# Performance work log

Hardware: AMD Instinct MI355X
Metric: run time of the kernel (lower is better)

## Reference

```python
import jax, jax.numpy as jnp
import numpy as np

B, L, P = 65536, 512, 96
E_LIN, E = 14, 16
FFT = 512
TEMP = 0.07
K = 2
EPS = 1e-5


def setup_inputs() -> dict:
    key = jax.random.key(0)
    k0, k1, k2 = jax.random.split(key, 3)
    x = jax.random.normal(k0, (B, L), dtype=jnp.float32)
    Wg = jax.random.normal(k1, (E, FFT // 2), dtype=jnp.float32) * 0.02
    bg = jnp.zeros((E,), dtype=jnp.float32)
    Wr = jax.random.normal(k2, (E_LIN, P, L), dtype=jnp.float32) * 0.02
    br = jnp.zeros((E_LIN, P), dtype=jnp.float32)
    return {"x": x, "Wg": Wg, "bg": bg, "Wr": Wr, "br": br}


def _periodogram(x):
    # x: [B, L] -> normalized power spectrum [B, FFT//2]
    x0 = x - jnp.mean(x, axis=1, keepdims=True)
    dft = jnp.fft.fft(x0, n=FFT, axis=1) / np.float32(np.sqrt(FFT))
    dft = dft[:, : FFT // 2]
    I = dft.real ** 2 + dft.imag ** 2
    s = jnp.sum(I, axis=1, keepdims=True)
    s = jnp.where(s == 0, jnp.ones_like(s), s)
    return I / s


def reference(x, Wg, bg, Wr, br):
    # gating (eval mode: no noise, divide by temperature)
    I = _periodogram(x)                                  # [B, F/2]
    gate = (I @ Wg.T + bg) / TEMP                        # [B, E]
    topv, topi = jax.lax.top_k(gate, K)                  # [B, K]
    gates = jax.nn.softmax(topv, axis=1)                 # [B, K]

    # RLinear experts: RevIN(norm) -> Linear -> RevIN(denorm); stats detached
    mu = jax.lax.stop_gradient(jnp.mean(x, axis=1, keepdims=True))        # [B,1]
    sd = jax.lax.stop_gradient(jnp.sqrt(jnp.var(x, axis=1, keepdims=True) + EPS))
    xn = (x - mu) / sd                                   # [B, L]
    yr = jnp.einsum('bl,epl->bep', xn, Wr) + br          # [B, E_LIN, P]
    yr = yr * sd[:, :, None] + mu[:, :, None]

    mean_out = jnp.broadcast_to(jnp.mean(x, axis=1, keepdims=True), (x.shape[0], P))[:, None, :]
    naive_out = jnp.broadcast_to(x[:, -1:], (x.shape[0], P))[:, None, :]

    eo = jnp.concatenate([yr, mean_out, naive_out], axis=1)   # [B, E, P]
    sel = jnp.take_along_axis(eo, topi[:, :, None], axis=1)   # [B, K, P]
    out = jnp.sum(gates[:, :, None] * sel, axis=1)            # [B, P]
    return out
```

## Files before the change

### kernel.cpp

```cpp
#include <hip/hip_runtime.h>
#include <math.h>

#define NB_B 65536
#define NL   512
#define NP   96
#define NE   16
#define NEL  14
#define NF   256
#define TEMP_INV (1.0f/0.07f)
#define TAU  1e-5f
#define PI_D 3.14159265358979323846
#define MAXCHK 1536

typedef __attribute__((ext_vector_type(8))) short bf16x8;
typedef __attribute__((ext_vector_type(4))) float f32x4;


#define WS_PCNT     0
#define WS_HOLES    16384
#define WS_PBASE    32768
#define WS_FLAGCNT  33792
#define WS_NCHK     33824
#define WS_HOLECNT  33840
#define WS_FLAG     33856
#define WS_SSUM     296000
#define WS_WGT      301376
#define WS_BGT      317760
#define WS_TWD      319872
#define WS_REC      328064
#define WS_HDR      590208
#define WS_RIDX     1638784
#define WS_WRB      1933696
#define WS_DESC     3506560
#define WS_XB16     3512704
#define WS_XB16_END 70621568

__device__ __forceinline__ unsigned short f2bf(float f) {
    unsigned u = __float_as_uint(f);
    unsigned r = (u + 0x7fffu + ((u >> 16) & 1u)) >> 16;
    return (unsigned short)r;
}

__global__ __launch_bounds__(256) void k_prep(
    const float* __restrict__ Wg, const float* __restrict__ bg,
    const float* __restrict__ Wr,
    float* __restrict__ Ssum, float* __restrict__ WgE, float* __restrict__ bgT,
    double2* __restrict__ twd,
    int* __restrict__ pcnt, int* __restrict__ flagcnt, int* __restrict__ holecnt,
    ushort4* __restrict__ Wrb, int perm)
{
    int g = blockIdx.x * 256 + threadIdx.x;
    {
        ushort4 o = make_ushort4(0, 0, 0, 0);
        if (g < NEL * NP * NL / 4) {
            float4 v;
            if (perm) {
                int row = g >> 7, sq = g & 127;
                int ll = sq >> 1, kb = (sq & 1) * 4;
                const float* wr = Wr + (size_t)row * NL + ll;
                v.x = wr[(kb + 0) * 64]; v.y = wr[(kb + 1) * 64];
                v.z = wr[(kb + 2) * 64]; v.w = wr[(kb + 3) * 64];
            } else {
                v = ((const float4*)Wr)[g];
            }
            o.x = f2bf(v.x); o.y = f2bf(v.y); o.z = f2bf(v.z); o.w = f2bf(v.w);
        }
        Wrb[g] = o;
    }
    if (g < NEL * NP * 8) {
        int row = g >> 3, seg = g & 7;
        const float4* w = (const float4*)(Wr + (size_t)row * NL + seg * 64);
        float s = 0.f;
#pragma unroll
        for (int i = 0; i < 16; i++) { float4 v = w[i]; s += v.x + v.y + v.z + v.w; }
        s += __shfl_xor(s, 1); s += __shfl_xor(s, 2); s += __shfl_xor(s, 4);
        if (seg == 0) Ssum[row] = s;
    }
    if (g < 4096) {
        int c = g & 3, e = (g >> 2) & 15, f4 = g >> 6;
        WgE[g] = Wg[e * NF + f4 * 4 + c] * TEMP_INV;
    }
    if (g < 512) {
        double a = -2.0 * PI_D * (double)g / 512.0;
        twd[g] = make_double2(cos(a), sin(a));
    }
    if (g < 256) pcnt[g << 4] = 0;
    if (g < NE) bgT[g] = bg[g] * TEMP_INV;
    if (g == 300) *flagcnt = 0;
    if (g == 301) *holecnt = 0;
}

__global__ __launch_bounds__(256, 4) void k_gate(
    const float* __restrict__ x,
    const float4* __restrict__ WgE4, const float* __restrict__ bgT,
    int* __restrict__ rec, float4* __restrict__ hdr,
    int* __restrict__ flaglist, int* __restrict__ flagcnt,
    int* __restrict__ pcnt, unsigned short* __restrict__ xb16, int bofs)
{
    __shared__ __align__(16) float2 s_z[4][576];
    float* s_Iv = (float*)&s_z[0][0];

    const int t = threadIdx.x;
    const int wv = t >> 6, l = t & 63;
    const int b0 = (bofs + blockIdx.x) * 8 + wv * 2;

    const float th = -6.283185307179586f / 512.0f;
    const float R2 = 0.70710678118654752f;
    float s1, c1; __sincosf((float)l * th, &s1, &c1);
    float s2, c2; __sincosf((float)(2 * l) * th, &s2, &c2);
    float sw0, cw0; __sincosf((float)((l & 31) << 3) * th, &sw0, &cw0);
    float sw1, cw1; __sincosf((float)((l & 15) << 4) * th, &sw1, &cw1);
    float sw2, cw2; __sincosf((float)((l & 7) << 5) * th, &sw2, &cw2);
    float2 tw0[4];
    tw0[0] = make_float2(c1, s1);
    tw0[1] = make_float2(R2 * (c1 + s1), R2 * (s1 - c1));
    tw0[2] = make_float2(s1, -c1);
    tw0[3] = make_float2(tw0[1].y, -tw0[1].x);
    float2 tw1[2];
    tw1[0] = make_float2(c2, s2);
    tw1[1] = make_float2(s2, -c2);
    const float2 w2 = make_float2(c2 * c2 - s2 * s2, 2.f * c2 * s2);
    float2 wst[5];
    wst[0] = make_float2(cw0, sw0);
    wst[1] = make_float2(cw1, sw1);
    wst[2] = make_float2(cw2, sw2);
    {
        int j2 = l & 3;
        float cc3 = (j2 == 0) ? 1.f : (j2 == 1) ? R2 : (j2 == 2) ? 0.f : -R2;
        float ss3 = (j2 == 0) ? 0.f : (j2 == 2) ? -1.f : -R2;
        wst[3] = make_float2(cc3, ss3);
    }
    wst[4] = (l & 1) ? make_float2(0.f, -1.f) : make_float2(1.f, 0.f);

    const float* xa = x + (size_t)b0 * NL;
    const float* xb = xa + NL;
    float xr[8], xi[8];
#pragma unroll
    for (int k = 0; k < 8; k++) { xr[k] = xa[k * 64 + l]; xi[k] = xb[k * 64 + l]; }
    const float last_a = __shfl(xr[7], 63);
    const float last_b = __shfl(xi[7], 63);

    if (xb16) {
        unsigned pa_[4], pb_[4];
#pragma unroll
        for (int j = 0; j < 4; j++) {
            asm("v_cvt_pk_bf16_f32 %0, %1, %2" : "=v"(pa_[j]) : "v"(xr[2 * j]), "v"(xr[2 * j + 1]));
            asm("v_cvt_pk_bf16_f32 %0, %1, %2" : "=v"(pb_[j]) : "v"(xi[2 * j]), "v"(xi[2 * j + 1]));
        }
        *(uint4*)(xb16 + (size_t)b0 * NL + l * 8)       = *(uint4*)pa_;
        *(uint4*)(xb16 + (size_t)(b0 + 1) * NL + l * 8) = *(uint4*)pb_;
    }

#pragma unroll
    for (int k = 0; k < 4; k++) {
        float2 w = tw0[k];
        float ur = xr[k], ui = xi[k], vr = xr[k + 4], vi = xi[k + 4];
        xr[k] = ur + vr; xi[k] = ui + vi;
        float dr = ur - vr, di = ui - vi;
        xr[k + 4] = dr * w.x - di * w.y; xi[k + 4] = dr * w.y + di * w.x;
    }
    {
        const int kk[4] = {0, 1, 4, 5};
#pragma unroll
        for (int g2 = 0; g2 < 4; g2++) {
            int k = kk[g2];
            float2 w = tw1[k & 1];
            float ur = xr[k], ui = xi[k], vr = xr[k + 2], vi = xi[k + 2];
            xr[k] = ur + vr; xi[k] = ui + vi;
            float dr = ur - vr, di = ui - vi;
            xr[k + 2] = dr * w.x - di * w.y; xi[k + 2] = dr * w.y + di * w.x;
        }
    }
    {
#pragma unroll
        for (int k = 0; k < 8; k += 2) {
            float ur = xr[k], ui = xi[k], vr = xr[k + 1], vi = xi[k + 1];
            xr[k] = ur + vr; xi[k] = ui + vi;
            float dr = ur - vr, di = ui - vi;
            xr[k + 1] = dr * w2.x - di * w2.y; xi[k + 1] = dr * w2.y + di * w2.x;
        }
    }
#pragma unroll
    for (int st = 3; st < 8; st++) {
        const int half = 256 >> st;
        const float2 w = wst[st - 3];
        const bool up = (l & half) != 0;
        const float sg = up ? -1.f : 1.f;
        const float cc = up ? w.x : 1.f;
        const float ss = up ? w.y : 0.f;
#pragma unroll
        for (int k = 0; k < 8; k++) {
            float pr = __shfl_xor(xr[k], half);
            float pi = __shfl_xor(xi[k], half);
            float tr = fmaf(sg, xr[k], pr);
            float ti = fmaf(sg, xi[k], pi);
            xr[k] = tr * cc - ti * ss;
            xi[k] = tr * ss + ti * cc;
        }
    }
    {
        const float sg = (l & 1) ? -1.f : 1.f;
#pragma unroll
        for (int k = 0; k < 8; k++) {
            float pr = __shfl_xor(xr[k], 1);
            float pi = __shfl_xor(xi[k], 1);
            xr[k] = fmaf(sg, xr[k], pr);
            xi[k] = fmaf(sg, xi[k], pi);
        }
    }

#pragma unroll
    for (int k = 0; k < 8; k++) {
        int i = k * 64 + l;
        s_z[wv][i + (i >> 3)] = make_float2(xr[k], xi[k]);
    }

    float Ia[4], Ib[4];
    float psa = 0.f, psb = 0.f;
#pragma unroll
    for (int j = 0; j < 4; j++) {
        int f = (l << 2) | j;
        int i1_ = (int)(__brev((unsigned)f) >> 23);
        int i2_ = (int)(__brev((unsigned)((512 - f) & 511)) >> 23);
        float2 z1 = s_z[wv][i1_ + (i1_ >> 3)];
        float2 z2 = s_z[wv][i2_ + (i2_ >> 3)];
        float pr_ = z1.x + z2.x, qm = z1.y - z2.y;
        float qp = z1.y + z2.y, pm = z1.x - z2.x;
        float va = pr_ * pr_ + qm * qm;
        float vb = qp * qp + pm * pm;
        if (f == 0) { va = 0.f; vb = 0.f; }
        Ia[j] = va; Ib[j] = vb;
        psa += va; psb += vb;
    }
#pragma unroll
    for (int m = 1; m < 64; m <<= 1) {
        psa += __shfl_xor(psa, m); psb += __shfl_xor(psb, m);
    }
    const float psa_raw = psa, psb_raw = psb;
    if (psa == 0.f) psa = 1.f;
    if (psb == 0.f) psb = 1.f;
    const float inv_a = 1.f / psa, inv_b = 1.f / psb;

    const float2 Z0   = s_z[wv][0];
    const float2 Z256 = s_z[wv][1];

    float* wI = s_Iv + wv * 1152;
    const int io = (l << 2) + ((l >> 4) << 2);
    *(float4*)(wI + io)       = make_float4(Ia[0], Ia[1], Ia[2], Ia[3]);
    *(float4*)(wI + 272 + io) = make_float4(Ib[0], Ib[1], Ib[2], Ib[3]);

    const int e16 = l & 15, cq = l >> 4;
    const float bgv = bgT[e16];
    float accA = 0.f, accB = 0.f;
    const float* rA = wI + cq * 68;
    const float* rB = rA + 272;
#pragma unroll 4
    for (int jj = 0; jj < 16; jj++) {
        float4 ia = *(const float4*)(rA + 4 * jj);
        float4 ib = *(const float4*)(rB + 4 * jj);
        float4 w = WgE4[(cq * 16 + jj) * 16 + e16];
        accA += ia.x * w.x + ia.y * w.y + ia.z * w.z + ia.w * w.w;
        accB += ib.x * w.x + ib.y * w.y + ib.z * w.z + ib.w * w.w;
    }
    accA += __shfl_xor(accA, 16); accA += __shfl_xor(accA, 32);
    accB += __shfl_xor(accB, 16); accB += __shfl_xor(accB, 32);

    float v = ((l & 16) ? accB * inv_b : accA * inv_a) + bgv;

    float b0v = v; int b0i = e16;
#pragma unroll
    for (int m = 1; m < 16; m <<= 1) {
        float ov = __shfl_xor(b0v, m); int oi = __shfl_xor(b0i, m);
        if (ov > b0v || (ov == b0v && oi < b0i)) { b0v = ov; b0i = oi; }
    }
    float v1 = (e16 == b0i) ? -1e30f : v;
    float b1v = v1; int b1i = e16;
#pragma unroll
    for (int m = 1; m < 16; m <<= 1) {
        float ov = __shfl_xor(b1v, m); int oi = __shfl_xor(b1i, m);
        if (ov > b1v || (ov == b1v && oi < b1i)) { b1v = ov; b1i = oi; }
    }
    float v2 = (e16 == b1i) ? -1e30f : v1;
    float b2v = v2;
#pragma unroll
    for (int m = 1; m < 16; m <<= 1) {
        float ov = __shfl_xor(b2v, m);
        b2v = fmaxf(b2v, ov);
    }

    if (l == 0 || l == 16) {
        const int r = l >> 4;
        const int b = b0 + r;
        const float mu = (r ? Z0.y : Z0.x) * (1.f / 512.f);
        const float Jv = r ? Z256.y : Z256.x;
        const float ps = r ? psb_raw : psa_raw;
        const float sd = sqrtf((0.5f * ps + Jv * Jv) * (1.f / 262144.f) + 1e-5f);
        const float last = r ? last_b : last_a;
        const float w0 = 1.f / (1.f + expf(b1v - b0v));
        const int pid = b0i * 16 + b1i;
        const int lo = atomicAdd(&pcnt[pid << 4], 1);
        rec[b] = (pid << 24) | lo;
        hdr[b] = make_float4(mu, sd, last, w0);
        if (b1v - b2v < TAU) {
            int pos = atomicAdd(flagcnt, 1);
            flaglist[pos] = b;
        }
    }
}

__global__ __launch_bounds__(256) void k_refine(
    const float* __restrict__ x, const double2* __restrict__ twd,
    const float* __restrict__ Wg, const float* __restrict__ bg,
    int* __restrict__ rec, float4* __restrict__ hdr,
    const int* __restrict__ flaglist, const int* __restrict__ flagcnt,
    int* __restrict__ pcnt, int* __restrict__ holes, int* __restrict__ holecnt)
{
    __shared__ double s_x[512];
    __shared__ double s_I[256];
    __shared__ double s_red[16];
    __shared__ double s_g[16];
    const int nf = *flagcnt;
    const int t = threadIdx.x;
    const int wid = t >> 6, lane = t & 63;
    for (int fi = blockIdx.x; fi < nf; fi += gridDim.x) {
        const int b = flaglist[fi];
        const float* xp = x + (size_t)b * NL;
        double v0 = (double)xp[t], v1 = (double)xp[t + 256];
        double lsum = v0 + v1;
        for (int m = 1; m < 64; m <<= 1) lsum += __shfl_xor(lsum, m);
        if (lane == 0) s_red[wid] = lsum;
        __syncthreads();
        double mu = (s_red[0] + s_red[1] + s_red[2] + s_red[3]) * (1.0 / 512.0);
        s_x[t] = v0 - mu; s_x[t + 256] = v1 - mu;
        __syncthreads();
        double2 w = twd[t];
        double pr = 1.0, pi = 0.0, cr = 0.0, ci = 0.0;
        for (int n = 0; n < 512; n++) {
            double xv = s_x[n];
            cr += xv * pr; ci += xv * pi;
            double t2 = pr * w.x - pi * w.y;
            pi = pr * w.y + pi * w.x;
            pr = t2;
        }
        double I = cr * cr + ci * ci;
        s_I[t] = I;
        double ls = I;
        for (int m = 1; m < 64; m <<= 1) ls += __shfl_xor(ls, m);
        if (lane == 0) s_red[8 + wid] = ls;
        __syncthreads();
        double stot = s_red[8] + s_red[9] + s_red[10] + s_red[11];
        if (stot == 0.0) stot = 1.0;
        if (t < 16) {
            double acc = 0.0;
            const float* wrow = Wg + t * NF;
            for (int f = 0; f < NF; f++) acc += s_I[f] * (double)wrow[f];
            s_g[t] = (acc / stot + (double)bg[t]) * (1.0 / 0.07);
        }
        __syncthreads();
        if (t == 0) {
            double c0 = -1e300, c1 = -1e300; int j0 = 0, j1 = 0;
            for (int i = 0; i < 16; i++) {
                double v = s_g[i];
                if (v > c0) { c1 = c0; j1 = j0; c0 = v; j0 = i; }
                else if (v > c1) { c1 = v; j1 = i; }
            }
            double e1 = exp(c1 - c0);
            float w0f = (float)(1.0 / (1.0 + e1));
            int newpid = j0 * 16 + j1;
            int oldrec = rec[b];
            int oldpid = (int)(((unsigned)oldrec) >> 24);
            if (newpid == oldpid) {
                ((float*)(hdr + b))[3] = w0f;
            } else {
                int pos = atomicAdd(holecnt, 1);
                if (pos < 4096) {
                    int nlo = atomicAdd(&pcnt[newpid << 4], 1);
                    rec[b] = (newpid << 24) | nlo;
                    holes[pos] = oldrec;
                    ((float*)(hdr + b))[3] = w0f;
                }
            }
        }
        __syncthreads();
    }
}

__global__ __launch_bounds__(256) void k_scan(
    const int* __restrict__ pcnt, int* __restrict__ pbase,
    int* __restrict__ desc, int* __restrict__ nchk)
{
    __shared__ int s[256], c[256];
    const int t = threadIdx.x;
    const int n = pcnt[t << 4];
    s[t] = n;
    c[t] = (n + 63) >> 6;
    __syncthreads();
    for (int off = 1; off < 256; off <<= 1) {
        int v1 = (t >= off) ? s[t - off] : 0;
        int v2 = (t >= off) ? c[t - off] : 0;
        __syncthreads();
        s[t] += v1; c[t] += v2;
        __syncthreads();
    }
    int excl = t ? s[t - 1] : 0;
    int cexcl = t ? c[t - 1] : 0;
    pbase[t] = excl;
    int myc = (n + 63) >> 6;
    for (int j = 0; j < myc; j++) desc[cexcl + j] = (t << 16) | j;
    if (t == 255) *nchk = cexcl + myc;
}

__global__ __launch_bounds__(256) void k_scatter(
    const int* __restrict__ rec, const int* __restrict__ pbase,
    int* __restrict__ ridx,
    const int* __restrict__ holes, const int* __restrict__ holecnt)
{
    const int t = threadIdx.x;
    const int b = blockIdx.x * 256 + t;
    unsigned v = (unsigned)rec[b];
    ridx[pbase[v >> 24] + (v & 0xFFFFFF)] = b;
    if (blockIdx.x == 0) {
        int nh = *holecnt; if (nh > 4096) nh = 4096;
        for (int h = t; h < nh; h += 256) {
            unsigned hv = (unsigned)holes[h];
            ridx[pbase[hv >> 24] + (hv & 0xFFFFFF)] = -1;
        }
    }
}

__global__ __launch_bounds__(256) void k_gemm2(
    const unsigned short* __restrict__ xb16,
    const unsigned short* __restrict__ Wrb,
    const float* __restrict__ br, const float* __restrict__ Ssum,
    const float4* __restrict__ hdr, float* __restrict__ out,
    const int* __restrict__ pcnt, const int* __restrict__ pbase,
    const int* __restrict__ ridx,
    const int* __restrict__ desc, const int* __restrict__ nchk)
{
    __shared__ __align__(16) unsigned short sB[2][2][96 * 68];
    __shared__ int    s_idx[64];
    __shared__ float4 s_hdr[64];
    __shared__ float  s_br[2][96], s_S[2][96];
    if ((int)blockIdx.x >= *nchk) return;
    const int d = desc[blockIdx.x];
    const int pid = d >> 16, cc = d & 0xffff;
    const int n = pcnt[pid << 4];
    const int base = pbase[pid];
    const int i0 = pid >> 4, i1 = pid & 15;
    const int t = threadIdx.x;
    const int lane = t & 63, wv = t >> 6;
    const int quad = lane >> 4, l16 = lane & 15;
    if (t < 96) {
        s_br[0][t] = (i0 < NEL) ? br[i0 * NP + t] : 0.f;
        s_S [0][t] = (i0 < NEL) ? Ssum[i0 * NP + t] : 0.f;
        s_br[1][t] = (i1 < NEL) ? br[i1 * NP + t] : 0.f;
        s_S [1][t] = (i1 < NEL) ? Ssum[i1 * NP + t] : 0.f;
    }
    if (t < 64) {
        int g = cc * 64 + t;
        bool vld = g < n;
        int row = vld ? ridx[base + g] : -1;
        s_idx[t] = row;
        s_hdr[t] = (row >= 0) ? hdr[row] : make_float4(0.f, 0.f, 0.f, 0.f);
    }

    const unsigned short* wb[2];
    wb[0] = Wrb + (size_t)i0 * NP * NL;
    wb[1] = Wrb + (size_t)i1 * NP * NL;
    unsigned boff[6]; int bpos[6], bex[6];
#pragma unroll
    for (int it = 0; it < 6; it++) {
        int ex = (it >= 3);
        int fl = t + (it - 3 * ex) * 256;
        int p = fl >> 3, kg = fl & 7;
        bex[it] = ex;
        boff[it] = (unsigned)(p * NL + kg * 8);
        bpos[it] = p * 68 + kg * 8;
    }

    bf16x8 bR[6];
#pragma unroll
    for (int it = 0; it < 6; it++) bR[it] = *(const bf16x8*)(wb[bex[it]] + boff[it]);
#pragma unroll
    for (int it = 0; it < 6; it++) *(bf16x8*)(&sB[0][bex[it]][bpos[it]]) = bR[it];
    __syncthreads();

    int arow = s_idx[wv * 16 + l16]; if (arow < 0) arow = 0;
    const unsigned short* aP = xb16 + (size_t)arow * NL + quad * 8;

    f32x4 acc[2][6];
#pragma unroll
    for (int ex = 0; ex < 2; ex++)
#pragma unroll
        for (int j = 0; j < 6; j++) acc[ex][j] = (f32x4){0.f, 0.f, 0.f, 0.f};

    bf16x8 a0 = *(const bf16x8*)(aP);
    bf16x8 a1 = *(const bf16x8*)(aP + 32);

    int cb = 0;
    for (int kb = 0; kb < NL; kb += 64) {
        const int kn = kb + 64;
        bf16x8 an0, an1;
        if (kn < NL) {
#pragma unroll
            for (int it = 0; it < 6; it++)
                bR[it] = *(const bf16x8*)(wb[bex[it]] + boff[it] + kn);
            an0 = *(const bf16x8*)(aP + kn);
            an1 = *(const bf16x8*)(aP + kn + 32);
        }
#pragma unroll
        for (int ks = 0; ks < 2; ks++)
#pragma unroll
            for (int ex = 0; ex < 2; ex++)
#pragma unroll
                for (int nt = 0; nt < 6; nt++) {
                    bf16x8 bf = *(const bf16x8*)(&sB[cb][ex][(nt * 16 + l16) * 68 + ks * 32 + quad * 8]);
                    acc[ex][nt] = __builtin_amdgcn_mfma_f32_16x16x32_bf16(
                        ks ? a1 : a0, bf, acc[ex][nt], 0, 0, 0);
                }
        if (kn < NL) {
#pragma unroll
            for (int it = 0; it < 6; it++) *(bf16x8*)(&sB[cb ^ 1][bex[it]][bpos[it]]) = bR[it];
            __syncthreads();
            cb ^= 1;
            a0 = an0; a1 = an1;
        }
    }

#pragma unroll
    for (int i = 0; i < 4; i++) {
        int rloc = wv * 16 + quad * 4 + i;
        int row = s_idx[rloc];
        if (row >= 0) {
            float4 h = s_hdr[rloc];
            float mu = h.x, sd = h.y, last = h.z, w0 = h.w, w1 = 1.f - w0;
            float* orow = out + (size_t)row * NP;
#pragma unroll
            for (int nt = 0; nt < 6; nt++) {
                int p = nt * 16 + l16;
                float v0 = (i0 < NEL) ? (mu + s_br[0][p] * sd - mu * s_S[0][p] + acc[0][nt][i])
                                      : (i0 == NEL ? mu : last);
                float v1 = (i1 < NEL) ? (mu + s_br[1][p] * sd - mu * s_S[1][p] + acc[1][nt][i])
                                      : (i1 == NEL ? mu : last);
                orow[p] = w0 * v0 + w1 * v1;
            }
        }
    }
}

__global__ __launch_bounds__(256) void k_gemm_f32(
    const float* __restrict__ x,
    const unsigned short* __restrict__ Wrb,
    const float* __restrict__ br, const float* __restrict__ Ssum,
    const float4* __restrict__ hdr, float* __restrict__ out,
    const int* __restrict__ pcnt, const int* __restrict__ pbase,
    const int* __restrict__ ridx,
    const int* __restrict__ desc, const int* __restrict__ nchk)
{
    __shared__ __align__(16) unsigned short sA[64 * 72];
    __shared__ __align__(16) unsigned short sB[2][96 * 72];
    __shared__ int    s_idx[64];
    __shared__ float4 s_hdr[64];
    __shared__ float  s_br[2][96], s_S[2][96];
    if ((int)blockIdx.x >= *nchk) return;
    const int d = desc[blockIdx.x];
    const int pid = d >> 16, cc = d & 0xffff;
    const int n = pcnt[pid << 4];
    const int base = pbase[pid];
    const int i0 = pid >> 4, i1 = pid & 15;
    const int t = threadIdx.x;
    const int lane = t & 63, wv = t >> 6;
    const int quad = lane >> 4, l16 = lane & 15;
    const int ar = t >> 2, asub = t & 3;
    if (t < 96) {
        s_br[0][t] = (i0 < NEL) ? br[i0 * NP + t] : 0.f;
        s_S [0][t] = (i0 < NEL) ? Ssum[i0 * NP + t] : 0.f;
        s_br[1][t] = (i1 < NEL) ? br[i1 * NP + t] : 0.f;
        s_S [1][t] = (i1 < NEL) ? Ssum[i1 * NP + t] : 0.f;
    }
    if (t < 64) {
        int g = cc * 64 + t;
        bool vld = g < n;
        int row = vld ? ridx[base + g] : -1;
        s_idx[t] = row;
        s_hdr[t] = (row >= 0) ? hdr[row] : make_float4(0.f, 0.f, 0.f, 0.f);
    }
    __syncthreads();

    f32x4 acc[2][6];
#pragma unroll
    for (int ex = 0; ex < 2; ex++)
#pragma unroll
        for (int j = 0; j < 6; j++) acc[ex][j] = (f32x4){0.f, 0.f, 0.f, 0.f};

    int rr = s_idx[ar]; if (rr < 0) rr = 0;

    unsigned boff[6];
    unsigned short* bdst[6];
    const unsigned short* wb[2];
    wb[0] = Wrb + (size_t)i0 * NP * NL;
    wb[1] = Wrb + (size_t)i1 * NP * NL;
    int bex[6];
#pragma unroll
    for (int it = 0; it < 6; it++) {
        int ex = (it >= 3);
        int fl = t + (it - 3 * ex) * 256;
        int p = fl >> 3, kg = fl & 7;
        bex[it] = ex;
        boff[it] = (unsigned)(p * NL + kg * 8);
        bdst[it] = &sB[ex][p * 72 + kg * 8];
    }
    unsigned short* adst = sA + ar * 72 + asub * 16;
    const float* xrowf = x + (size_t)rr * NL + asub * 16;

    float4 fA[4]; bf16x8 bR[6];
#pragma unroll
    for (int i = 0; i < 4; i++) fA[i] = ((const float4*)xrowf)[i];
#pragma unroll
    for (int it = 0; it < 6; it++) bR[it] = *(const bf16x8*)(wb[bex[it]] + boff[it]);

    for (int kb = 0; kb < NL; kb += 64) {
        unsigned short tmp[16];
#pragma unroll
        for (int i = 0; i < 4; i++) {
            float4 v = fA[i];
            tmp[i * 4 + 0] = f2bf(v.x); tmp[i * 4 + 1] = f2bf(v.y);
            tmp[i * 4 + 2] = f2bf(v.z); tmp[i * 4 + 3] = f2bf(v.w);
        }
        *(bf16x8*)adst       = *(bf16x8*)tmp;
        *(bf16x8*)(adst + 8) = *(bf16x8*)(tmp + 8);
#pragma unroll
        for (int it = 0; it < 6; it++) *(bf16x8*)bdst[it] = bR[it];
        __syncthreads();

        const int kn = kb + 64;
        if (kn < NL) {
#pragma unroll
            for (int i = 0; i < 4; i++) fA[i] = ((const float4*)(xrowf + kn))[i];
#pragma unroll
            for (int it = 0; it < 6; it++)
                bR[it] = *(const bf16x8*)(wb[bex[it]] + boff[it] + kn);
        }

#pragma unroll
        for (int ks = 0; ks < 2; ks++) {
            bf16x8 af = *(const bf16x8*)(sA + (wv * 16 + l16) * 72 + ks * 32 + quad * 8);
#pragma unroll
            for (int ex = 0; ex < 2; ex++)
#pragma unroll
                for (int nt = 0; nt < 6; nt++) {
                    bf16x8 bf = *(const bf16x8*)(&sB[ex][(nt * 16 + l16) * 72 + ks * 32 + quad * 8]);
                    acc[ex][nt] = __builtin_amdgcn_mfma_f32_16x16x32_bf16(af, bf, acc[ex][nt], 0, 0, 0);
                }
        }
        __syncthreads();
    }
#pragma unroll
    for (int i = 0; i < 4; i++) {
        int rloc = wv * 16 + quad * 4 + i;
        int row = s_idx[rloc];
        if (row >= 0) {
            float4 h = s_hdr[rloc];
            float mu = h.x, sd = h.y, last = h.z, w0 = h.w, w1 = 1.f - w0;
            float* orow = out + (size_t)row * NP;
#pragma unroll
            for (int nt = 0; nt < 6; nt++) {
                int p = nt * 16 + l16;
                float v0 = (i0 < NEL) ? (mu + s_br[0][p] * sd - mu * s_S[0][p] + acc[0][nt][i])
                                      : (i0 == NEL ? mu : last);
                float v1 = (i1 < NEL) ? (mu + s_br[1][p] * sd - mu * s_S[1][p] + acc[1][nt][i])
                                      : (i1 == NEL ? mu : last);
                orow[p] = w0 * v0 + w1 * v1;
            }
        }
    }
}

extern "C" void kernel_launch(void* const* d_in, const int* in_sizes, int n_in,
                              void* d_out, int out_size, void* d_ws, size_t ws_size,
                              hipStream_t stream)
{
    const float* x  = (const float*)d_in[0];
    const float* Wg = (const float*)d_in[1];
    const float* bg = (const float*)d_in[2];
    const float* Wr = (const float*)d_in[3];
    const float* br = (const float*)d_in[4];
    float* out = (float*)d_out;
    char* ws = (char*)d_ws;

    int*     pcnt     = (int*)(ws + WS_PCNT);
    int*     holes    = (int*)(ws + WS_HOLES);
    int*     pbase    = (int*)(ws + WS_PBASE);
    int*     flagcnt  = (int*)(ws + WS_FLAGCNT);
    int*     nchk     = (int*)(ws + WS_NCHK);
    int*     holecnt  = (int*)(ws + WS_HOLECNT);
    int*     flaglist = (int*)(ws + WS_FLAG);
    float*   Ssum     = (float*)(ws + WS_SSUM);
    float*   WgE      = (float*)(ws + WS_WGT);
    float*   bgT      = (float*)(ws + WS_BGT);
    double2* twd      = (double2*)(ws + WS_TWD);
    int*     rec      = (int*)(ws + WS_REC);
    float4*  hdr      = (float4*)(ws + WS_HDR);
    int*     ridx     = (int*)(ws + WS_RIDX);
    unsigned short* Wrb = (unsigned short*)(ws + WS_WRB);
    int*     desc     = (int*)(ws + WS_DESC);

    const int use_xb = (ws_size >= (size_t)WS_XB16_END);
    unsigned short* xb16 = use_xb ? (unsigned short*)(ws + WS_XB16) : (unsigned short*)0;

    k_prep<<<dim3(768), dim3(256), 0, stream>>>(Wg, bg, Wr, Ssum, WgE, bgT, twd,
                                                pcnt, flagcnt, holecnt,
                                                (ushort4*)Wrb, use_xb);
    k_gate<<<dim3(NB_B / 16), dim3(256), 0, stream>>>(x, (const float4*)WgE, bgT,
                                                      rec, hdr, flaglist, flagcnt, pcnt,
                                                      xb16, 0);
    k_gate<<<dim3(NB_B / 16), dim3(256), 0, stream>>>(x, (const float4*)WgE, bgT,
                                                      rec, hdr, flaglist, flagcnt, pcnt,
                                                      xb16, NB_B / 16);
    k_refine<<<dim3(512), dim3(256), 0, stream>>>(x, twd, Wg, bg, rec, hdr,
                                                  flaglist, flagcnt, pcnt, holes, holecnt);
    k_scan<<<dim3(1), dim3(256), 0, stream>>>(pcnt, pbase, desc, nchk);
    k_scatter<<<dim3(NB_B / 256), dim3(256), 0, stream>>>(rec, pbase, ridx, holes, holecnt);
    if (use_xb)
        k_gemm2<<<dim3(MAXCHK), dim3(256), 0, stream>>>(xb16, Wrb, br, Ssum, hdr, out,
                                                        pcnt, pbase, ridx, desc, nchk);
    else
        k_gemm_f32<<<dim3(MAXCHK), dim3(256), 0, stream>>>(x, Wrb, br, Ssum, hdr, out,
                                                           pcnt, pbase, ridx, desc, nchk);
}
```

Baseline: 306.7 us.

## Single-buffer gemm LDS, XCD-aware block remap, nontemporal loads/stores, merge gate launches

The grouped expert GEMM drops LDS double buffering in favour of a single buffer per expert, halving shared memory at the cost of an extra barrier per k-step. Chunk indices are remapped so consecutive descriptors spread across the 8 XCDs. Activation, header and output accesses use nontemporal hints to avoid polluting cache. The two half-batch gate launches are fused into one launch.

```diff
diff --git a/kernel.cpp b/kernel.cpp
--- a/kernel.cpp
+++ b/kernel.cpp
@@ -14,6 +14,7 @@
 
 typedef __attribute__((ext_vector_type(8))) short bf16x8;
 typedef __attribute__((ext_vector_type(4))) float f32x4;
+typedef __attribute__((ext_vector_type(4))) unsigned int u32x4;
 
 
 #define WS_PCNT     0
@@ -39,6 +40,14 @@
     unsigned u = __float_as_uint(f);
     unsigned r = (u + 0x7fffu + ((u >> 16) & 1u)) >> 16;
     return (unsigned short)r;
+}
+__device__ __forceinline__ bf16x8 ldnt_bf16x8(const unsigned short* p) {
+    u32x4 v = __builtin_nontemporal_load((const u32x4*)p);
+    union { u32x4 u; bf16x8 h; } c; c.u = v; return c.h;
+}
+__device__ __forceinline__ float4 ldnt_f4(const float4* p) {
+    u32x4 v = __builtin_nontemporal_load((const u32x4*)p);
+    union { u32x4 u; float4 f; } c; c.u = v; return c.f;
 }
 
 __global__ __launch_bounds__(256) void k_prep(
@@ -95,14 +104,14 @@
     const float4* __restrict__ WgE4, const float* __restrict__ bgT,
     int* __restrict__ rec, float4* __restrict__ hdr,
     int* __restrict__ flaglist, int* __restrict__ flagcnt,
-    int* __restrict__ pcnt, unsigned short* __restrict__ xb16, int bofs)
+    int* __restrict__ pcnt, unsigned short* __restrict__ xb16)
 {
     __shared__ __align__(16) float2 s_z[4][576];
     float* s_Iv = (float*)&s_z[0][0];
 
     const int t = threadIdx.x;
     const int wv = t >> 6, l = t & 63;
-    const int b0 = (bofs + blockIdx.x) * 8 + wv * 2;
+    const int b0 = blockIdx.x * 8 + wv * 2;
 
     const float th = -6.283185307179586f / 512.0f;
     const float R2 = 0.70710678118654752f;
@@ -428,7 +437,7 @@
     }
 }
 
-__global__ __launch_bounds__(256) void k_gemm2(
+__global__ __launch_bounds__(256) void k_gemm3(
     const unsigned short* __restrict__ xb16,
     const unsigned short* __restrict__ Wrb,
     const float* __restrict__ br, const float* __restrict__ Ssum,
@@ -437,12 +446,13 @@
     const int* __restrict__ ridx,
     const int* __restrict__ desc, const int* __restrict__ nchk)
 {
-    __shared__ __align__(16) unsigned short sB[2][2][96 * 68];
+    __shared__ __align__(16) unsigned short sB[2][96 * 68];
     __shared__ int    s_idx[64];
     __shared__ float4 s_hdr[64];
     __shared__ float  s_br[2][96], s_S[2][96];
-    if ((int)blockIdx.x >= *nchk) return;
-    const int d = desc[blockIdx.x];
+    const int lb = (int)(blockIdx.x % 8) * (MAXCHK / 8) + (int)(blockIdx.x / 8);
+    if (lb >= *nchk) return;
+    const int d = desc[lb];
     const int pid = d >> 16, cc = d & 0xffff;
     const int n = pcnt[pid << 4];
     const int base = pbase[pid];
@@ -461,7 +471,7 @@
         bool vld = g < n;
         int row = vld ? ridx[base + g] : -1;
         s_idx[t] = row;
-        s_hdr[t] = (row >= 0) ? hdr[row] : make_float4(0.f, 0.f, 0.f, 0.f);
+        s_hdr[t] = (row >= 0) ? ldnt_f4(hdr + row) : make_float4(0.f, 0.f, 0.f, 0.f);
     }
 
     const unsigned short* wb[2];
@@ -481,8 +491,6 @@
     bf16x8 bR[6];
 #pragma unroll
     for (int it = 0; it < 6; it++) bR[it] = *(const bf16x8*)(wb[bex[it]] + boff[it]);
-#pragma unroll
-    for (int it = 0; it < 6; it++) *(bf16x8*)(&sB[0][bex[it]][bpos[it]]) = bR[it];
     __syncthreads();
 
     int arow = s_idx[wv * 16 + l16]; if (arow < 0) arow = 0;
@@ -494,35 +502,36 @@
 #pragma unroll
         for (int j = 0; j < 6; j++) acc[ex][j] = (f32x4){0.f, 0.f, 0.f, 0.f};
 
-    bf16x8 a0 = *(const bf16x8*)(aP);
-    bf16x8 a1 = *(const bf16x8*)(aP + 32);
-
-    int cb = 0;
+    bf16x8 a0 = ldnt_bf16x8(aP);
+    bf16x8 a1 = ldnt_bf16x8(aP + 32);
+
     for (int kb = 0; kb < NL; kb += 64) {
+#pragma unroll
+        for (int it = 0; it < 6; it++) *(bf16x8*)(&sB[bex[it]][bpos[it]]) = bR[it];
+        __syncthreads();
+
         const int kn = kb + 64;
         bf16x8 an0, an1;
         if (kn < NL) {
 #pragma unroll
             for (int it = 0; it < 6; it++)
                 bR[it] = *(const bf16x8*)(wb[bex[it]] + boff[it] + kn);
-            an0 = *(const bf16x8*)(aP + kn);
-            an1 = *(const bf16x8*)(aP + kn + 32);
-        }
+            an0 = ldnt_bf16x8(aP + kn);
+            an1 = ldnt_bf16x8(aP + kn + 32);
+        }
+
 #pragma unroll
         for (int ks = 0; ks < 2; ks++)
 #pragma unroll
             for (int ex = 0; ex < 2; ex++)
 #pragma unroll
                 for (int nt = 0; nt < 6; nt++) {
-                    bf16x8 bf = *(const bf16x8*)(&sB[cb][ex][(nt * 16 + l16) * 68 + ks * 32 + quad * 8]);
+                    bf16x8 bf = *(const bf16x8*)(&sB[ex][(nt * 16 + l16) * 68 + ks * 32 + quad * 8]);
                     acc[ex][nt] = __builtin_amdgcn_mfma_f32_16x16x32_bf16(
                         ks ? a1 : a0, bf, acc[ex][nt], 0, 0, 0);
                 }
         if (kn < NL) {
-#pragma unroll
-            for (int it = 0; it < 6; it++) *(bf16x8*)(&sB[cb ^ 1][bex[it]][bpos[it]]) = bR[it];
             __syncthreads();
-            cb ^= 1;
             a0 = an0; a1 = an1;
         }
     }
@@ -542,7 +551,7 @@
                                       : (i0 == NEL ? mu : last);
                 float v1 = (i1 < NEL) ? (mu + s_br[1][p] * sd - mu * s_S[1][p] + acc[1][nt][i])
                                       : (i1 == NEL ? mu : last);
-                orow[p] = w0 * v0 + w1 * v1;
+                __builtin_nontemporal_store(w0 * v0 + w1 * v1, &orow[p]);
             }
         }
     }
@@ -711,18 +720,14 @@
     k_prep<<<dim3(768), dim3(256), 0, stream>>>(Wg, bg, Wr, Ssum, WgE, bgT, twd,
                                                 pcnt, flagcnt, holecnt,
                                                 (ushort4*)Wrb, use_xb);
-    k_gate<<<dim3(NB_B / 16), dim3(256), 0, stream>>>(x, (const float4*)WgE, bgT,
-                                                      rec, hdr, flaglist, flagcnt, pcnt,
-                                                      xb16, 0);
-    k_gate<<<dim3(NB_B / 16), dim3(256), 0, stream>>>(x, (const float4*)WgE, bgT,
-                                                      rec, hdr, flaglist, flagcnt, pcnt,
-                                                      xb16, NB_B / 16);
+    k_gate<<<dim3(NB_B / 8), dim3(256), 0, stream>>>(x, (const float4*)WgE, bgT,
+                                                     rec, hdr, flaglist, flagcnt, pcnt, xb16);
     k_refine<<<dim3(512), dim3(256), 0, stream>>>(x, twd, Wg, bg, rec, hdr,
                                                   flaglist, flagcnt, pcnt, holes, holecnt);
     k_scan<<<dim3(1), dim3(256), 0, stream>>>(pcnt, pbase, desc, nchk);
     k_scatter<<<dim3(NB_B / 256), dim3(256), 0, stream>>>(rec, pbase, ridx, holes, holecnt);
     if (use_xb)
-        k_gemm2<<<dim3(MAXCHK), dim3(256), 0, stream>>>(xb16, Wrb, br, Ssum, hdr, out,
+        k_gemm3<<<dim3(MAXCHK), dim3(256), 0, stream>>>(xb16, Wrb, br, Ssum, hdr, out,
                                                         pcnt, pbase, ridx, desc, nchk);
     else
         k_gemm_f32<<<dim3(MAXCHK), dim3(256), 0, stream>>>(x, Wrb, br, Ssum, hdr, out,
```

Measured after the change: 304.4 us. About the same (-0.8%).
